# Performance work log

Measured on AMD Instinct MI355X. Metric: run time of the kernel, lower is better.

Reference implementation:

```python
import jax, jax.numpy as jnp
import numpy as np

N_NODES = 100000
N_EDGES = 1600000
NUM_GRAPHS = 4096
EPS = 1e-5


def _glorot(key, shape):
    fan_in, fan_out = shape[0], shape[1]
    lim = float(np.sqrt(6.0 / (fan_in + fan_out)))
    return jax.random.uniform(key, shape, jnp.float32, -lim, lim)


def setup_inputs() -> dict:
    key = jax.random.key(0)
    ks = jax.random.split(key, 32)
    inp = {}
    inp['x'] = jax.random.normal(ks[0], (N_NODES, 32), jnp.float32)
    inp['edge_attr'] = jax.random.uniform(ks[1], (N_EDGES, 8), jnp.float32)
    inp['edge_index'] = jax.random.randint(ks[2], (2, N_EDGES), 0, N_NODES, jnp.int32)
    inp['batch'] = jnp.sort(jax.random.randint(ks[3], (N_NODES,), 0, NUM_GRAPHS, jnp.int32))
    inp['num_graphs'] = NUM_GRAPHS
    # node/edge embeddings
    inp['Wn'] = _glorot(ks[4], (32, 64)); inp['bn_'] = jnp.zeros((64,), jnp.float32)
    inp['We'] = _glorot(ks[5], (8, 16)); inp['be_'] = jnp.zeros((16,), jnp.float32)
    # conv1: 2*64+16=144 -> 128 -> 64
    inp['W1a'] = _glorot(ks[6], (144, 128)); inp['b1a'] = jnp.zeros((128,), jnp.float32)
    inp['W1b'] = _glorot(ks[7], (128, 64)); inp['b1b'] = jnp.zeros((64,), jnp.float32)
    # conv2: 2*64+16=144 -> 64 -> 32
    inp['W2a'] = _glorot(ks[8], (144, 64)); inp['b2a'] = jnp.zeros((64,), jnp.float32)
    inp['W2b'] = _glorot(ks[9], (64, 32)); inp['b2b'] = jnp.zeros((32,), jnp.float32)
    # conv3: 2*32+16=80 -> 32 -> 16
    inp['W3a'] = _glorot(ks[10], (80, 32)); inp['b3a'] = jnp.zeros((32,), jnp.float32)
    inp['W3b'] = _glorot(ks[11], (32, 16)); inp['b3b'] = jnp.zeros((16,), jnp.float32)
    # batchnorm affine params
    inp['g1'] = jnp.ones((64,), jnp.float32); inp['beta1'] = jnp.zeros((64,), jnp.float32)
    inp['g2'] = jnp.ones((32,), jnp.float32); inp['beta2'] = jnp.zeros((32,), jnp.float32)
    inp['g3'] = jnp.ones((16,), jnp.float32); inp['beta3'] = jnp.zeros((16,), jnp.float32)
    # final fc 16 -> 12
    inp['Wfc'] = _glorot(ks[12], (16, 12)); inp['bfc'] = jnp.zeros((12,), jnp.float32)
    return inp


def _conv(x, e_emb, src, dst, Wa, ba, Wb, bb, n_nodes):
    # PyG: x_i = x[target]=x[dst], x_j = x[source]=x[src]; message MLP; mean-aggregate at dst
    m = jnp.concatenate([x[dst], x[src], e_emb], axis=1)      # [E, 2*in+edge]
    m = jax.nn.relu(m @ Wa + ba) @ Wb + bb                    # [E, out]
    s = jax.ops.segment_sum(m, dst, num_segments=n_nodes)
    cnt = jax.ops.segment_sum(jnp.ones((m.shape[0], 1), m.dtype), dst, num_segments=n_nodes)
    return s / jnp.maximum(cnt, 1.0)


def _batchnorm(x, g, b):
    mu = jnp.mean(x, axis=0)
    var = jnp.mean(jnp.square(x - mu), axis=0)
    return (x - mu) * jax.lax.rsqrt(var + EPS) * g + b


def reference(x, edge_attr, edge_index, batch, num_graphs,
              Wn, bn_, We, be_, W1a, b1a, W1b, b1b, W2a, b2a, W2b, b2b,
              W3a, b3a, W3b, b3b, g1, beta1, g2, beta2, g3, beta3, Wfc, bfc):
    n_nodes = x.shape[0]
    src, dst = edge_index[0], edge_index[1]
    e_emb = jax.nn.relu(edge_attr @ We + be_)                 # [E, 16]
    h = jax.nn.relu(x @ Wn + bn_)                             # [N, 64]
    h = _conv(h, e_emb, src, dst, W1a, b1a, W1b, b1b, n_nodes)
    h = jax.nn.relu(_batchnorm(h, g1, beta1))
    h = _conv(h, e_emb, src, dst, W2a, b2a, W2b, b2b, n_nodes)
    h = jax.nn.relu(_batchnorm(h, g2, beta2))
    h = _conv(h, e_emb, src, dst, W3a, b3a, W3b, b3b, n_nodes)
    h = jax.nn.relu(_batchnorm(h, g3, beta3))
    # global mean pool per graph
    s = jax.ops.segment_sum(h, batch, num_segments=num_graphs)
    cnt = jax.ops.segment_sum(jnp.ones((n_nodes, 1), h.dtype), batch, num_segments=num_graphs)
    pooled = s / jnp.maximum(cnt, 1.0)                        # [G, 16]
    return jax.nn.sigmoid(pooled @ Wfc + bfc)                 # [G, 12]
```

## Files before the change

### kernel.cpp

```cpp
#include <hip/hip_runtime.h>
#include <hip/hip_bf16.h>
#include <cstdio>


#define N_NODES 100000
#define N_EDGES 1600000
#define NUM_GRAPHS 4096

typedef unsigned short u16;
typedef unsigned int u32;
typedef _Float16 h2 __attribute__((ext_vector_type(2)));

#if defined(__has_builtin)
#if __has_builtin(__builtin_amdgcn_fdot2)
#define DOT2(a, b, c) __builtin_amdgcn_fdot2((a), (b), (c), false)
#endif
#endif
#ifndef DOT2
#define DOT2(a, b, c) ((c) + (float)(a).x * (float)(b).x + (float)(a).y * (float)(b).y)
#endif

__device__ __forceinline__ float b2f(u16 u) { union { u32 i; float f; } c; c.i = ((u32)u) << 16; return c.f; }
__device__ __forceinline__ float b2f_lo(u32 u) { union { u32 i; float f; } c; c.i = u << 16; return c.f; }
__device__ __forceinline__ float b2f_hi(u32 u) { union { u32 i; float f; } c; c.i = u & 0xffff0000u; return c.f; }
__device__ __forceinline__ u16 f2b(float f) {
    __hip_bfloat16 h = __float2bfloat16(f);
    return *reinterpret_cast<u16*>(&h);
}

template <int CPL>
__device__ __forceinline__ void ld_bf16(const u16* base, float out[CPL]) {
    if constexpr (CPL == 1) {
        out[0] = b2f(*base);
    } else {
        u32 v = *(const u32*)base;
        out[0] = b2f_lo(v); out[1] = b2f_hi(v);
    }
}
template <int CPL>
__device__ __forceinline__ void ld_f32(const float* base, float out[CPL]) {
    if constexpr (CPL == 1) {
        out[0] = *base;
    } else {
        float2 v = *(const float2*)base;
        out[0] = v.x; out[1] = v.y;
    }
}

__global__ __launch_bounds__(256) void hist_k(const int* __restrict__ dst, int* __restrict__ hist) {
    int e = blockIdx.x * 256 + threadIdx.x;
    if (e < N_EDGES) atomicAdd(&hist[dst[e]], 1);
}

__global__ __launch_bounds__(256) void scan_part_k(const int* __restrict__ hist,
        int* __restrict__ excl, int* __restrict__ bsum) {
    __shared__ int sm[256];
    int t = threadIdx.x, b = blockIdx.x;
    int base = b * 1024 + t * 4;
    int v0 = (base + 0 < N_NODES) ? hist[base + 0] : 0;
    int v1 = (base + 1 < N_NODES) ? hist[base + 1] : 0;
    int v2 = (base + 2 < N_NODES) ? hist[base + 2] : 0;
    int v3 = (base + 3 < N_NODES) ? hist[base + 3] : 0;
    int tsum = v0 + v1 + v2 + v3;
    sm[t] = tsum;
    __syncthreads();
    for (int o = 1; o < 256; o <<= 1) {
        int x = (t >= o) ? sm[t - o] : 0;
        __syncthreads();
        sm[t] += x;
        __syncthreads();
    }
    int texcl = sm[t] - tsum;
    if (base + 0 < N_NODES) excl[base + 0] = texcl;
    if (base + 1 < N_NODES) excl[base + 1] = texcl + v0;
    if (base + 2 < N_NODES) excl[base + 2] = texcl + v0 + v1;
    if (base + 3 < N_NODES) excl[base + 3] = texcl + v0 + v1 + v2;
    if (t == 255) bsum[b] = sm[255];
}

__global__ __launch_bounds__(256) void scan_top_k(int* __restrict__ bsum, int* __restrict__ boff,
        int nb, int* __restrict__ row_ptr_last) {
    __shared__ int sm[256];
    int t = threadIdx.x;
    int v = (t < nb) ? bsum[t] : 0;
    sm[t] = v;
    __syncthreads();
    for (int o = 1; o < 256; o <<= 1) {
        int x = (t >= o) ? sm[t - o] : 0;
        __syncthreads();
        sm[t] += x;
        __syncthreads();
    }
    if (t < nb) boff[t] = sm[t] - v;
    if (t == 0) *row_ptr_last = sm[255];
}

__global__ __launch_bounds__(256) void scan_add_k(int* __restrict__ excl, const int* __restrict__ boff,
        int* __restrict__ row_ptr, int* __restrict__ cursor) {
    int i = blockIdx.x * 256 + threadIdx.x;
    if (i >= N_NODES) return;
    int s = excl[i] + boff[i >> 10];
    row_ptr[i] = s;
    cursor[i] = s;
}

__global__ __launch_bounds__(256) void scatter_k(const int* __restrict__ src, const int* __restrict__ dst,
        int* __restrict__ cursor, int2* __restrict__ epk) {
    int e = blockIdx.x * 256 + threadIdx.x;
    if (e < N_EDGES) {
        int p = atomicAdd(&cursor[dst[e]], 1);
        int2 q; q.x = src[e]; q.y = e;
        epk[p] = q;
    }
}

__global__ __launch_bounds__(256) void ubound_k(const int* __restrict__ row_ptr, int* __restrict__ sn) {
    int u = blockIdx.x * 256 + threadIdx.x;
    if (u > 25000) return;
    if (u == 25000) { sn[u] = N_NODES; return; }
    int target = u * 64;
    int lo = 0, hi = N_NODES;
    while (lo < hi) {
        int mid = (lo + hi) >> 1;
        if (row_ptr[mid] >= target) hi = mid; else lo = mid + 1;
    }
    sn[u] = lo;
}

__global__ __launch_bounds__(256) void edge_emb_k(const float* __restrict__ ea,
        const float* __restrict__ We, const float* __restrict__ be,
        const int2* __restrict__ epk, _Float16* __restrict__ e16s) {
    int idx = blockIdx.x * 256 + threadIdx.x;
    int p = idx >> 4, k = idx & 15;
    int e = epk[p].y;
    float4 a0 = *(const float4*)(ea + (size_t)e * 8);
    float4 a1 = *(const float4*)(ea + (size_t)e * 8 + 4);
    float acc = be[k];
    acc += a0.x * We[0 * 16 + k];
    acc += a0.y * We[1 * 16 + k];
    acc += a0.z * We[2 * 16 + k];
    acc += a0.w * We[3 * 16 + k];
    acc += a1.x * We[4 * 16 + k];
    acc += a1.y * We[5 * 16 + k];
    acc += a1.z * We[6 * 16 + k];
    acc += a1.w * We[7 * 16 + k];
    e16s[(size_t)idx] = (_Float16)fmaxf(acc, 0.f);
}

__global__ __launch_bounds__(256) void node_emb2_k(const float* __restrict__ x,
        const float* __restrict__ Wn, const float* __restrict__ bn_, float* __restrict__ h) {
    constexpr int C = 64, F = 32, TILE = 64;
    __shared__ float xs[TILE * F];
    const int t = threadIdx.x;
    const int grp = t / C;
    const int c = t % C;
    float w[F];
#pragma unroll
    for (int k = 0; k < F; ++k) w[k] = Wn[(size_t)k * 64 + c];
    const float bias = bn_[c];
    const float4* xsrc = (const float4*)x;
    float4* xs4 = (float4*)xs;

    for (int v0 = blockIdx.x * TILE; v0 < N_NODES; v0 += gridDim.x * TILE) {
        __syncthreads();
        for (int i = t; i < TILE * F / 4; i += 256) {
            int vv = v0 + (i * 4) / F;
            float4 val;
            if (vv < N_NODES) val = xsrc[(size_t)v0 * (F / 4) + i];
            else { val.x = val.y = val.z = val.w = 0.f; }
            xs4[i] = val;
        }
        __syncthreads();
        const int base = grp * 16;
        const int nmax = (N_NODES - v0 - base >= 16) ? 16
                        : (N_NODES - v0 - base > 0 ? N_NODES - v0 - base : 0);
        for (int n = 0; n < nmax; ++n) {
            const int v = v0 + base + n;
            const float4* xr4 = (const float4*)&xs[(base + n) * F];
            float a0 = bias, a1 = 0.f, a2 = 0.f, a3 = 0.f;
#pragma unroll
            for (int k4 = 0; k4 < F / 4; ++k4) {
                float4 hv = xr4[k4];
                a0 += hv.x * w[4 * k4 + 0];
                a1 += hv.y * w[4 * k4 + 1];
                a2 += hv.z * w[4 * k4 + 2];
                a3 += hv.w * w[4 * k4 + 3];
            }
            h[(size_t)v * 64 + c] = fmaxf((a0 + a1) + (a2 + a3), 0.f);
        }
    }
}

template <int F, int H, bool BN>
__global__ __launch_bounds__(256) void proj_k(const float* __restrict__ h,
        const float* __restrict__ Wa, const float* __restrict__ ba,
        const float* __restrict__ stats, const float* __restrict__ g, const float* __restrict__ beta,
        float* __restrict__ Pd, u16* __restrict__ Ps) {
    constexpr int C2 = 2 * H;
    constexpr int NPB = 256 / C2;
    constexpr int TILE = 16 * NPB;
    __shared__ float hs[TILE][F];
    __shared__ float sc[BN ? F : 1];
    __shared__ float shv[BN ? F : 1];
    const int t = threadIdx.x;
    if constexpr (BN) {
        if (t < F) {
            const float invN = 1.0f / (float)N_NODES;
            float mu = stats[t] * invN;
            float ex2 = stats[F + t] * invN;
            float var = fmaxf(ex2 - mu * mu, 0.f);
            float rs = rsqrtf(var + 1e-5f);
            float scale = rs * g[t];
            sc[t] = scale;
            shv[t] = beta[t] - mu * scale;
        }
    }
    const int grp = t / C2;
    const int c = t % C2;
    const bool is_src = (c >= H);
    const int cc = is_src ? (c - H) : c;
    float w[F];
    const float* wcol = Wa + (size_t)(is_src ? F : 0) * H + cc;
#pragma unroll
    for (int k = 0; k < F; ++k) w[k] = wcol[(size_t)k * H];
    const float bias = is_src ? 0.f : ba[cc];

    for (int v0 = blockIdx.x * TILE; v0 < N_NODES; v0 += gridDim.x * TILE) {
        __syncthreads();
        for (int i = t; i < TILE * F; i += 256) {
            int vv = v0 + i / F;
            float val = (vv < N_NODES) ? h[(size_t)vv * F + (i % F)] : 0.f;
            if constexpr (BN) val = fmaxf(val * sc[i % F] + shv[i % F], 0.f);
            hs[i / F][i % F] = val;
        }
        __syncthreads();
        const int base = grp * 16;
        const int nmax = (N_NODES - v0 - base >= 16) ? 16
                        : (N_NODES - v0 - base > 0 ? N_NODES - v0 - base : 0);
#pragma unroll 2
        for (int n = 0; n < nmax; ++n) {
            const int v = v0 + base + n;
            const float4* hr4 = (const float4*)hs[base + n];
            float a0 = bias, a1 = 0.f, a2 = 0.f, a3 = 0.f;
#pragma unroll
            for (int k4 = 0; k4 < F / 4; ++k4) {
                float4 hv = hr4[k4];
                a0 += hv.x * w[4 * k4 + 0];
                a1 += hv.y * w[4 * k4 + 1];
                a2 += hv.z * w[4 * k4 + 2];
                a3 += hv.w * w[4 * k4 + 3];
            }
            float acc = (a0 + a1) + (a2 + a3);
            if (is_src) Ps[(size_t)v * H + cc] = f2b(acc);
            else        Pd[(size_t)v * H + cc] = acc;
        }
    }
}

template <int H>
__global__ __launch_bounds__(256) void conv_k(
        const int* __restrict__ sn, const int* __restrict__ row_ptr,
        const int2* __restrict__ epk, const _Float16* __restrict__ e16s,
        float* __restrict__ Pd, const u16* __restrict__ Ps,
        const float* __restrict__ Wae) {
    constexpr int SL = (H >= 64) ? 64 : 32;
    constexpr int NPW = 64 / SL;
    constexpr int CPL = H / SL;
    const int wave = threadIdx.x >> 6, lane = threadIdx.x & 63;
    const int sub = lane / SL;
    const int sl = lane % SL;
    const int c0 = sl * CPL;
    h2 w2h[8][CPL];
#pragma unroll
    for (int k2 = 0; k2 < 8; ++k2)
#pragma unroll
        for (int j = 0; j < CPL; ++j) {
            h2 t;
            t.x = (_Float16)Wae[(2 * k2) * H + c0 + j];
            t.y = (_Float16)Wae[(2 * k2 + 1) * H + c0 + j];
            w2h[k2][j] = t;
        }

    const int uid = (blockIdx.x * 4 + wave) * NPW + sub;
    const int vbeg = sn[uid], vend = sn[uid + 1];

    for (int v = vbeg; v < vend; ++v) {
        const int vv = (SL == 64) ? __builtin_amdgcn_readfirstlane(v) : v;
        float pd[CPL], acc[CPL];
        ld_f32<CPL>(&Pd[(size_t)vv * H + c0], pd);
#pragma unroll
        for (int j = 0; j < CPL; ++j) acc[j] = 0.f;
        const int p0 = row_ptr[vv], p1 = row_ptr[vv + 1];
        const int deg = p1 - p0;

        auto edge = [&](uint4 ra, uint4 rb, const float ps[CPL]) {
            union { u32 u; h2 h; } cv;
            h2 ev[8];
            cv.u = ra.x; ev[0] = cv.h; cv.u = ra.y; ev[1] = cv.h;
            cv.u = ra.z; ev[2] = cv.h; cv.u = ra.w; ev[3] = cv.h;
            cv.u = rb.x; ev[4] = cv.h; cv.u = rb.y; ev[5] = cv.h;
            cv.u = rb.z; ev[6] = cv.h; cv.u = rb.w; ev[7] = cv.h;
            float z[CPL];
#pragma unroll
            for (int j = 0; j < CPL; ++j) z[j] = pd[j] + ps[j];
#pragma unroll
            for (int k2 = 0; k2 < 8; ++k2)
#pragma unroll
                for (int j = 0; j < CPL; ++j) z[j] = DOT2(ev[k2], w2h[k2][j], z[j]);
#pragma unroll
            for (int j = 0; j < CPL; ++j) acc[j] += fmaxf(z[j], 0.f);
        };

        int p = p0;
        for (; p + 3 < p1; p += 4) {
            int2 q0 = epk[p], q1 = epk[p + 1], q2 = epk[p + 2], q3 = epk[p + 3];
            const uint4* e0 = (const uint4*)(e16s + (size_t)p * 16);
            uint4 a0 = e0[0], a1 = e0[1];
            uint4 b0 = e0[2], b1 = e0[3];
            uint4 g0 = e0[4], g1 = e0[5];
            uint4 d0 = e0[6], d1 = e0[7];
            float ps0[CPL], ps1[CPL], ps2[CPL], ps3[CPL];
            ld_bf16<CPL>(&Ps[(size_t)q0.x * H + c0], ps0);
            ld_bf16<CPL>(&Ps[(size_t)q1.x * H + c0], ps1);
            ld_bf16<CPL>(&Ps[(size_t)q2.x * H + c0], ps2);
            ld_bf16<CPL>(&Ps[(size_t)q3.x * H + c0], ps3);
            edge(a0, a1, ps0);
            edge(b0, b1, ps1);
            edge(g0, g1, ps2);
            edge(d0, d1, ps3);
        }
        for (; p < p1; ++p) {
            int2 q0 = epk[p];
            const uint4* e0 = (const uint4*)(e16s + (size_t)p * 16);
            uint4 a0 = e0[0], a1 = e0[1];
            float ps0[CPL];
            ld_bf16<CPL>(&Ps[(size_t)q0.x * H + c0], ps0);
            edge(a0, a1, ps0);
        }

        const float invd = (deg > 0) ? 1.f / (float)deg : 0.f;
        if constexpr (CPL == 2) {
            float2 o; o.x = acc[0] * invd; o.y = acc[1] * invd;
            *(float2*)&Pd[(size_t)vv * H + c0] = o;
        } else {
            Pd[(size_t)vv * H + c0] = acc[0] * invd;
        }
    }
}

template <int H, int Fo>
__global__ __launch_bounds__(256) void matvec2_k(const float* __restrict__ m,
        const int* __restrict__ row_ptr,
        const float* __restrict__ Wb, const float* __restrict__ bb,
        float* __restrict__ y, float* __restrict__ stats) {
    constexpr int FoC = (Fo < 32) ? Fo : 32;
    constexpr int CG = Fo / FoC;
    constexpr int NPW = 32 / FoC;
    constexpr int NG = 4 / CG;
    constexpr int SLOTS = NG * NPW;
    constexpr int KH = H / 2;
    constexpr int TILE = 4096 / H;
    constexpr int J = TILE / SLOTS;

    __shared__ float hs[TILE * H];
    __shared__ int ptile[TILE + 1];
    __shared__ float sh[2 * Fo];

    const int t = threadIdx.x;
    const int wave = t >> 6, lane = t & 63;
    const int kh = lane >> 5;
    const int r = lane & 31;
    const int c_lo = r % FoC;
    const int s = r / FoC;
    const int cg = wave % CG;
    const int ng = wave / CG;
    const int c = cg * FoC + c_lo;
    const int slot = ng * NPW + s;

    for (int i = t; i < 2 * Fo; i += 256) sh[i] = 0.f;

    float w[KH];
#pragma unroll
    for (int k = 0; k < KH; ++k) w[k] = Wb[(size_t)(kh * KH + k) * Fo + c];
    const float bias = bb[c];
    float s1 = 0.f, s2 = 0.f;

    const float4* msrc = (const float4*)m;
    float4* hs4 = (float4*)hs;

    for (int v0 = blockIdx.x * TILE; v0 < N_NODES; v0 += gridDim.x * TILE) {
        __syncthreads();
#pragma unroll
        for (int q = t; q < 1024; q += 256) {
            int node = (q * 4) / H;
            float4 val;
            if (v0 + node < N_NODES) val = msrc[(size_t)v0 * (H / 4) + q];
            else { val.x = val.y = val.z = val.w = 0.f; }
            hs4[q] = val;
        }
        for (int i = t; i <= TILE; i += 256) {
            int v = v0 + i;
            ptile[i] = row_ptr[v < N_NODES ? v : N_NODES];
        }
        __syncthreads();

        for (int j = 0; j < J; ++j) {
            const int n = slot + j * SLOTS;
            const int v = v0 + n;
            const float4* hr4 = (const float4*)&hs[n * H + kh * KH];
            float a0 = 0.f, a1 = 0.f, a2 = 0.f, a3 = 0.f;
#pragma unroll
            for (int k4 = 0; k4 < KH / 4; ++k4) {
                float4 hv = hr4[k4];
                a0 += hv.x * w[4 * k4 + 0];
                a1 += hv.y * w[4 * k4 + 1];
                a2 += hv.z * w[4 * k4 + 2];
                a3 += hv.w * w[4 * k4 + 3];
            }
            float half = (a0 + a1) + (a2 + a3);
            float total = half + __shfl_xor(half, 32) + bias;
            if (kh == 0 && v < N_NODES) {
                const int deg = ptile[n + 1] - ptile[n];
                float val = (deg > 0) ? total : 0.f;
                y[(size_t)v * Fo + c] = val;
                s1 += val; s2 += val * val;
            }
        }
    }

    __syncthreads();
    if (kh == 0) {
        atomicAdd(&sh[c], s1);
        atomicAdd(&sh[Fo + c], s2);
    }
    __syncthreads();
    if (t < 2 * Fo) atomicAdd(&stats[t], sh[t]);
}

__global__ __launch_bounds__(256) void pool_bn_k(const float* __restrict__ y,
        const float* __restrict__ stats, const float* __restrict__ g, const float* __restrict__ beta,
        const int* __restrict__ batch, float* __restrict__ pool, int* __restrict__ gcnt) {
    int idx = blockIdx.x * 256 + threadIdx.x;
    if (idx >= N_NODES * 16) return;
    int v = idx >> 4, c = idx & 15;
    const float invN = 1.0f / (float)N_NODES;
    float mu = stats[c] * invN;
    float ex2 = stats[16 + c] * invN;
    float var = fmaxf(ex2 - mu * mu, 0.f);
    float rs = rsqrtf(var + 1e-5f);
    float val = fmaxf((y[idx] - mu) * rs * g[c] + beta[c], 0.f);
    int b = batch[v];
    atomicAdd(&pool[b * 16 + c], val);
    if (c == 0) atomicAdd(&gcnt[b], 1);
}

__global__ __launch_bounds__(256) void out_k(const float* __restrict__ pool,
        const int* __restrict__ gcnt, const float* __restrict__ Wfc,
        const float* __restrict__ bfc, float* __restrict__ out) {
    int idx = blockIdx.x * 256 + threadIdx.x;
    if (idx >= NUM_GRAPHS * 12) return;
    int g = idx / 12, o = idx % 12;
    int cnt = gcnt[g];
    float inv = 1.0f / (float)(cnt > 0 ? cnt : 1);
    float acc = bfc[o];
#pragma unroll
    for (int k = 0; k < 16; ++k) acc += pool[g * 16 + k] * inv * Wfc[k * 12 + o];
    out[idx] = 1.0f / (1.0f + expf(-acc));
}

extern "C" void kernel_launch(void* const* d_in, const int* in_sizes, int n_in,
                              void* d_out, int out_size, void* d_ws, size_t ws_size,
                              hipStream_t stream) {
    const size_t N = N_NODES, E = N_EDGES, G = NUM_GRAPHS;
    const float* x = (const float*)d_in[0];
    const float* ea = (const float*)d_in[1];
    const int* ei = (const int*)d_in[2];
    const int* srcv = ei;
    const int* dstv = ei + E;
    const int* batch = (const int*)d_in[3];
    const float* Wn = (const float*)d_in[5];  const float* bn_ = (const float*)d_in[6];
    const float* We = (const float*)d_in[7];  const float* be_ = (const float*)d_in[8];
    const float* W1a = (const float*)d_in[9]; const float* b1a = (const float*)d_in[10];
    const float* W1b = (const float*)d_in[11]; const float* b1b = (const float*)d_in[12];
    const float* W2a = (const float*)d_in[13]; const float* b2a = (const float*)d_in[14];
    const float* W2b = (const float*)d_in[15]; const float* b2b = (const float*)d_in[16];
    const float* W3a = (const float*)d_in[17]; const float* b3a = (const float*)d_in[18];
    const float* W3b = (const float*)d_in[19]; const float* b3b = (const float*)d_in[20];
    const float* g1 = (const float*)d_in[21]; const float* be1 = (const float*)d_in[22];
    const float* g2 = (const float*)d_in[23]; const float* be2 = (const float*)d_in[24];
    const float* g3 = (const float*)d_in[25]; const float* be3 = (const float*)d_in[26];
    const float* Wfc = (const float*)d_in[27]; const float* bfc = (const float*)d_in[28];

    char* base = (char*)d_ws;
    size_t off = 0;
    auto take = [&](size_t bytes) { size_t o = off; off += (bytes + 255) & ~(size_t)255; return o; };
    int* hist = (int*)(base + take(N * 4));
    int* cursor = (int*)(base + take(N * 4));
    int* row_ptr = (int*)(base + take((N + 1) * 4));
    int* bsum = (int*)(base + take(256 * 4));
    int* boff = (int*)(base + take(256 * 4));
    int* sn = (int*)(base + take(25001 * 4));
    int2* epk = (int2*)(base + take(E * 8));
    float* hbuf = (float*)(base + take(N * 64 * 4));
    float* Pd = (float*)(base + take(N * 128 * 4));
    u16* Ps = (u16*)(base + take(N * 128 * 2));
    _Float16* e16s = (_Float16*)(base + take(E * 16 * 2));
    float* stats = (float*)(base + take(256 * 4));
    float* pool = (float*)(base + take(G * 16 * 4));
    int* gcnt = (int*)(base + take(G * 4));
    if (off > ws_size) {
        fprintf(stderr, "kernel_launch: ws too small: need %zu have %zu\n", off, ws_size);
        return;
    }

    const int NB = (N_NODES + 1023) / 1024;

    hipMemsetAsync(hist, 0, N * 4, stream);
    hist_k<<<dim3((E + 255) / 256), dim3(256), 0, stream>>>(dstv, hist);
    scan_part_k<<<dim3(NB), dim3(256), 0, stream>>>(hist, cursor, bsum);
    scan_top_k<<<dim3(1), dim3(256), 0, stream>>>(bsum, boff, NB, &row_ptr[N_NODES]);
    scan_add_k<<<dim3((N + 255) / 256), dim3(256), 0, stream>>>(cursor, boff, row_ptr, cursor);
    scatter_k<<<dim3((E + 255) / 256), dim3(256), 0, stream>>>(srcv, dstv, cursor, epk);
    ubound_k<<<dim3((25001 + 255) / 256), dim3(256), 0, stream>>>(row_ptr, sn);

    edge_emb_k<<<dim3(E * 16 / 256), dim3(256), 0, stream>>>(ea, We, be_, epk, e16s);
    node_emb2_k<<<dim3(1563), dim3(256), 0, stream>>>(x, Wn, bn_, hbuf);

    proj_k<64, 128, false><<<dim3(6250), dim3(256), 0, stream>>>(hbuf, W1a, b1a, nullptr, nullptr, nullptr, Pd, Ps);
    conv_k<128><<<dim3(6250), dim3(256), 0, stream>>>(sn, row_ptr, epk, e16s, Pd, Ps, W1a + 128 * 128);
    hipMemsetAsync(stats, 0, 256 * 4, stream);
    matvec2_k<128, 64><<<dim3(1024), dim3(256), 0, stream>>>(Pd, row_ptr, W1b, b1b, hbuf, stats);

    proj_k<64, 64, true><<<dim3(3125), dim3(256), 0, stream>>>(hbuf, W2a, b2a, stats, g1, be1, Pd, Ps);
    conv_k<64><<<dim3(6250), dim3(256), 0, stream>>>(sn, row_ptr, epk, e16s, Pd, Ps, W2a + 128 * 64);
    hipMemsetAsync(stats, 0, 256 * 4, stream);
    matvec2_k<64, 32><<<dim3(1024), dim3(256), 0, stream>>>(Pd, row_ptr, W2b, b2b, hbuf, stats);

    proj_k<32, 32, true><<<dim3(1563), dim3(256), 0, stream>>>(hbuf, W3a, b3a, stats, g2, be2, Pd, Ps);
    conv_k<32><<<dim3(3125), dim3(256), 0, stream>>>(sn, row_ptr, epk, e16s, Pd, Ps, W3a + 64 * 32);
    hipMemsetAsync(stats, 0, 256 * 4, stream);
    matvec2_k<32, 16><<<dim3(1024), dim3(256), 0, stream>>>(Pd, row_ptr, W3b, b3b, hbuf, stats);

    hipMemsetAsync(pool, 0, G * 16 * 4, stream);
    hipMemsetAsync(gcnt, 0, G * 4, stream);
    pool_bn_k<<<dim3((N * 16 + 255) / 256), dim3(256), 0, stream>>>(hbuf, stats, g3, be3, batch, pool, gcnt);
    out_k<<<dim3((G * 12 + 255) / 256), dim3(256), 0, stream>>>(pool, gcnt, Wfc, bfc, (float*)d_out);
}
```

Measured before the change: 1.014 ms.

## Replace atomic CSR scatter with two-pass bucketed counting sort

The single-pass scatter, which did one global atomic per edge on a random destination cursor, is replaced by a two-level counting sort. Edges are first routed into 512-node buckets using shared-memory histograms and one global atomic per bucket per chunk. A per-bucket kernel then places each edge at its final CSR slot using shared-memory cursors. This cuts contended global atomics and random 8-byte writes, at the cost of an extra temporary E-sized buffer and an additional read/write pass.

```diff
diff --git a/kernel.cpp b/kernel.cpp
--- a/kernel.cpp
+++ b/kernel.cpp
@@ -6,6 +6,9 @@
 #define N_NODES 100000
 #define N_EDGES 1600000
 #define NUM_GRAPHS 4096
+#define BK_SH 9
+#define NBK ((N_NODES + 511) >> 9)
+#define CHUNK 4096
 
 typedef unsigned short u16;
 typedef unsigned int u32;
@@ -96,21 +99,67 @@
 }
 
 __global__ __launch_bounds__(256) void scan_add_k(int* __restrict__ excl, const int* __restrict__ boff,
-        int* __restrict__ row_ptr, int* __restrict__ cursor) {
+        int* __restrict__ row_ptr) {
     int i = blockIdx.x * 256 + threadIdx.x;
     if (i >= N_NODES) return;
-    int s = excl[i] + boff[i >> 10];
-    row_ptr[i] = s;
-    cursor[i] = s;
-}
-
-__global__ __launch_bounds__(256) void scatter_k(const int* __restrict__ src, const int* __restrict__ dst,
-        int* __restrict__ cursor, int2* __restrict__ epk) {
-    int e = blockIdx.x * 256 + threadIdx.x;
-    if (e < N_EDGES) {
-        int p = atomicAdd(&cursor[dst[e]], 1);
-        int2 q; q.x = src[e]; q.y = e;
-        epk[p] = q;
+    row_ptr[i] = excl[i] + boff[i >> 10];
+}
+
+__global__ __launch_bounds__(256) void bucketcur_k(const int* __restrict__ row_ptr, int* __restrict__ bcur) {
+    int b = blockIdx.x * 256 + threadIdx.x;
+    if (b < NBK) bcur[b] = row_ptr[b << BK_SH];
+}
+
+__global__ __launch_bounds__(256) void route_k(const int* __restrict__ src, const int* __restrict__ dst,
+        int* __restrict__ bcur, int2* __restrict__ tmp) {
+    __shared__ int hcnt[NBK];
+    __shared__ int hbase[NBK];
+    const int t = threadIdx.x;
+    const int e0 = blockIdx.x * CHUNK;
+    const int e1 = (e0 + CHUNK < N_EDGES) ? e0 + CHUNK : N_EDGES;
+    for (int i = t; i < NBK; i += 256) hcnt[i] = 0;
+    __syncthreads();
+    for (int e = e0 + t; e < e1; e += 256)
+        atomicAdd(&hcnt[dst[e] >> BK_SH], 1);
+    __syncthreads();
+    for (int i = t; i < NBK; i += 256) {
+        int c = hcnt[i];
+        hbase[i] = (c > 0) ? atomicAdd(&bcur[i], c) : 0;
+        hcnt[i] = 0;
+    }
+    __syncthreads();
+    for (int e = e0 + t; e < e1; e += 256) {
+        int d = dst[e];
+        int b = d >> BK_SH;
+        int r = atomicAdd(&hcnt[b], 1);
+        int2 q;
+        q.x = src[e];
+        q.y = e | ((d & 511) << 21);
+        tmp[hbase[b] + r] = q;
+    }
+}
+
+__global__ __launch_bounds__(256) void fine_k(const int* __restrict__ row_ptr,
+        const int2* __restrict__ tmp, int2* __restrict__ epk) {
+    __shared__ int cur[512];
+    const int t = threadIdx.x;
+    const int b = blockIdx.x;
+    const int n0 = b << BK_SH;
+    for (int i = t; i < 512; i += 256) {
+        int n = n0 + i;
+        cur[i] = row_ptr[(n < N_NODES) ? n : N_NODES];
+    }
+    __syncthreads();
+    const int nEnd = (n0 + 512 < N_NODES) ? n0 + 512 : N_NODES;
+    const int p0 = row_ptr[n0], p1 = row_ptr[nEnd];
+    for (int i = p0 + t; i < p1; i += 256) {
+        int2 q = tmp[i];
+        int dl = (q.y >> 21) & 511;
+        int pos = atomicAdd(&cur[dl], 1);
+        int2 o;
+        o.x = q.x;
+        o.y = q.y & 0x1FFFFF;
+        epk[pos] = o;
     }
 }
 
@@ -495,12 +544,14 @@
     size_t off = 0;
     auto take = [&](size_t bytes) { size_t o = off; off += (bytes + 255) & ~(size_t)255; return o; };
     int* hist = (int*)(base + take(N * 4));
-    int* cursor = (int*)(base + take(N * 4));
+    int* excl = (int*)(base + take(N * 4));
     int* row_ptr = (int*)(base + take((N + 1) * 4));
     int* bsum = (int*)(base + take(256 * 4));
     int* boff = (int*)(base + take(256 * 4));
+    int* bcur = (int*)(base + take(256 * 4));
     int* sn = (int*)(base + take(25001 * 4));
     int2* epk = (int2*)(base + take(E * 8));
+    int2* tmp = (int2*)(base + take(E * 8));
     float* hbuf = (float*)(base + take(N * 64 * 4));
     float* Pd = (float*)(base + take(N * 128 * 4));
     u16* Ps = (u16*)(base + take(N * 128 * 2));
@@ -517,10 +568,12 @@
 
     hipMemsetAsync(hist, 0, N * 4, stream);
     hist_k<<<dim3((E + 255) / 256), dim3(256), 0, stream>>>(dstv, hist);
-    scan_part_k<<<dim3(NB), dim3(256), 0, stream>>>(hist, cursor, bsum);
+    scan_part_k<<<dim3(NB), dim3(256), 0, stream>>>(hist, excl, bsum);
     scan_top_k<<<dim3(1), dim3(256), 0, stream>>>(bsum, boff, NB, &row_ptr[N_NODES]);
-    scan_add_k<<<dim3((N + 255) / 256), dim3(256), 0, stream>>>(cursor, boff, row_ptr, cursor);
-    scatter_k<<<dim3((E + 255) / 256), dim3(256), 0, stream>>>(srcv, dstv, cursor, epk);
+    scan_add_k<<<dim3((N + 255) / 256), dim3(256), 0, stream>>>(excl, boff, row_ptr);
+    bucketcur_k<<<dim3(1), dim3(256), 0, stream>>>(row_ptr, bcur);
+    route_k<<<dim3((N_EDGES + CHUNK - 1) / CHUNK), dim3(256), 0, stream>>>(srcv, dstv, bcur, tmp);
+    fine_k<<<dim3(NBK), dim3(256), 0, stream>>>(row_ptr, tmp, epk);
     ubound_k<<<dim3((25001 + 255) / 256), dim3(256), 0, stream>>>(row_ptr, sn);
 
     edge_emb_k<<<dim3(E * 16 / 256), dim3(256), 0, stream>>>(ea, We, be_, epk, e16s);
```

Result: faster. 942.7 us (-7.0%).
